# Kernel tuning notes

Measured on AMD Instinct MI355X. Metric: run time of the kernel, lower is better.

## Reference

```python
import jax, jax.numpy as jnp
import numpy as np

D = 2            # stalk dimension d
FD = 3           # final_d = d + 1 (add_lp=True, add_hp=False)
HID = 32         # hidden_channels
N_NODES = 50000
E0 = 200000      # undirected edges; directed edge list has 2*E0 entries (second half reversed)
IN_CH = 128
OUT_CH = 32
N_LAYERS = 2
PSIZE = D * (D + 1) // 2  # cayley param size per edge


def _spectral_normalize(W, iters=20):
    # torch spectral_norm: power iteration with detached u, v; sigma = u^T W v
    u = jnp.full((W.shape[0],), 1.0 / np.sqrt(W.shape[0]), W.dtype)
    def body(_, u):
        v = W.T @ u
        v = v / (jnp.linalg.norm(v) + 1e-12)
        u2 = W @ v
        return u2 / (jnp.linalg.norm(u2) + 1e-12)
    u = jax.lax.fori_loop(0, iters, body, u)
    u = jax.lax.stop_gradient(u)
    v = jax.lax.stop_gradient(W.T @ u)
    v = v / (jnp.linalg.norm(v) + 1e-12)
    return W / (u @ W @ v)


def _cayley(p):
    # p: [E, PSIZE] lower-tri params -> skew A -> orthogonal Q = (I - A)^{-1}(I + A)
    E = p.shape[0]
    r, c = jnp.tril_indices(D)
    M = jnp.zeros((E, D, D), p.dtype).at[:, r, c].set(p)
    A = M - jnp.swapaxes(M, 1, 2)
    I = jnp.eye(D, dtype=p.dtype)
    return jnp.linalg.solve(I[None] - A, I[None] + A)


def setup_inputs() -> dict:
    key = jax.random.key(0)
    ks = jax.random.split(key, 8)
    src = jax.random.randint(ks[0], (E0,), 0, N_NODES)
    dst = jax.random.randint(ks[1], (E0,), 0, N_NODES)
    # symmetric directed edge list; edge j and edge j+E0 are reverses of each other
    edge_index = jnp.concatenate([jnp.stack([src, dst]), jnp.stack([dst, src])], axis=1)
    x = jax.random.normal(ks[2], (N_NODES, IN_CH), jnp.float32)
    s = 0.02
    W1 = jax.random.normal(ks[3], (FD * HID, IN_CH), jnp.float32) * s
    b1 = jnp.zeros((FD * HID,), jnp.float32)
    W2 = jax.random.normal(ks[4], (OUT_CH, FD * HID), jnp.float32) * s
    b2 = jnp.zeros((OUT_CH,), jnp.float32)
    W_left = jnp.tile(jnp.eye(FD, dtype=jnp.float32)[None], (N_LAYERS, 1, 1))  # init eye per torch
    W_right = jax.random.normal(ks[5], (N_LAYERS, HID, HID), jnp.float32) / np.sqrt(HID)
    eps = jnp.zeros((N_LAYERS, FD, 1), jnp.float32)
    W_sheaf = jax.random.normal(ks[6], (N_LAYERS, PSIZE, 2 * FD * HID), jnp.float32) * s
    W_wt = jax.random.normal(ks[7], (N_LAYERS, 1, 2 * FD * HID), jnp.float32) * s
    return {"x": x, "edge_index": edge_index, "W1": W1, "b1": b1, "W2": W2, "b2": b2,
            "W_left": W_left, "W_right": W_right, "eps": eps, "W_sheaf": W_sheaf, "W_wt": W_wt}


def reference(x, edge_index, W1, b1, W2, b2, W_left, W_right, eps, W_sheaf, W_wt):
    N = x.shape[0]
    row, col = edge_index[0], edge_index[1]
    e0 = row.shape[0] // 2
    rev = jnp.concatenate([jnp.arange(e0) + e0, jnp.arange(e0)])  # reverse-edge index
    # lin1 + ELU (dropouts = 0 in eval)
    h = jax.nn.elu(x @ W1.T + b1)                 # [N, FD*HID]
    xc = h.reshape(N * FD, HID)                   # [N*FD, HID]
    x0 = xc
    for layer in range(N_LAYERS):
        # --- sheaf learner + edge weight learner (gather endpoint features) ---
        xn = xc.reshape(N, FD * HID)
        cat = jnp.concatenate([xn[row], xn[col]], axis=-1)   # [2*E0, 2*FD*HID]
        p = jnp.tanh(cat @ W_sheaf[layer].T)                 # sheaf map params [2*E0, PSIZE]
        wdir = jax.nn.sigmoid(cat @ W_wt[layer].T)[:, 0]
        w = wdir * wdir[rev]                                 # symmetric edge weight
        # --- normalized connection (bundle) Laplacian ---
        Q = _cayley(p)                                       # per-edge orthogonal maps
        T = jnp.einsum('eij,eik->ejk', Q, Q[rev])            # transport F_u^T F_v
        w2 = w * w
        deg = jax.ops.segment_sum(w2, row, num_segments=N)
        dinv = jnp.where(deg > 0, jax.lax.rsqrt(jnp.maximum(deg, 1e-30)), 0.0)
        cnorm = w2 * dinv[row] * dinv[col]                   # [2*E0]
        # --- left / right weights (spectral-normalized) ---
        Wl = _spectral_normalize(W_left[layer])
        Wr = _spectral_normalize(W_right[layer])
        y = xc.reshape(N, FD, HID)
        y = jnp.einsum('ef,nfh->neh', Wl, y)                 # mix stalk dims
        y = jnp.einsum('neh,ch->nec', y, Wr)                 # mix channels
        # --- apply block-sparse Laplacian: Lx[u] = x[u] - sum_e c_e B_e x[v] ---
        yv = y[col]                                          # gather  [2*E0, FD, HID]
        tv = jnp.concatenate([jnp.einsum('eij,ejh->eih', T, yv[:, :D]), yv[:, D:]], axis=1)
        agg = jax.ops.segment_sum(cnorm[:, None, None] * tv, row, num_segments=N)
        diag = jnp.where(deg > 0, 1.0, 0.0)[:, None, None]
        z = jax.nn.elu((diag * y - agg).reshape(N * FD, HID))
        # --- epsilon-gated residual ---
        coeff = jnp.tile(1.0 + jnp.tanh(eps[layer]), (N, 1))  # [N*FD, 1]
        x0 = coeff * x0 - z
        xc = x0
    return xc.reshape(N, FD * HID) @ W2.T + b2
```

## Files before the change

kernel.cpp:

```cpp
#include <hip/hip_runtime.h>

#define NN 50000
#define E0 200000
#define E2 400000
#define NGROUPS ((NN + 7) / 8)
#define NCHUNK  ((NN + 255) / 256)
#define NTILES  ((NN + 63) / 64)

typedef __attribute__((ext_vector_type(8))) short short8;
typedef __attribute__((ext_vector_type(4))) float f32x4;

__device__ __forceinline__ float eluf(float x) { return x > 0.0f ? x : expm1f(x); }
__device__ __forceinline__ float sigmoidf(float x) { return 1.0f / (1.0f + expf(-x)); }
__device__ __forceinline__ unsigned rne_bf16(float x) {
    unsigned u = __float_as_uint(x);
    return (u + 0x7fffu + ((u >> 16) & 1u)) >> 16;
}

__global__ __launch_bounds__(256) void k_setup(const float* __restrict__ W1, const float* __restrict__ W2,
                                               const float* __restrict__ Wl_in, const float* __restrict__ Wr_in,
                                               float* __restrict__ Wl_out, float* __restrict__ Wr_out,
                                               unsigned short* __restrict__ w1hi, unsigned short* __restrict__ w1lo,
                                               unsigned short* __restrict__ w2hi, unsigned short* __restrict__ w2lo,
                                               int* __restrict__ cnt, int* __restrict__ fill,
                                               float* __restrict__ deg) {
    __shared__ float W[32 * 33];
    __shared__ float us[32], vs[32], tmp[32];
    __shared__ float scal;
    int t = threadIdx.x;
    if (blockIdx.x < 2) {
        int l = blockIdx.x;
        for (int i = t; i < 1024; i += 256) W[(i >> 5) * 33 + (i & 31)] = Wr_in[l * 1024 + i];
        if (t < 32) us[t] = 0.17677669529663688f;
        __syncthreads();
        for (int it = 0; it < 20; ++it) {
            if (t < 32) { float a = 0; for (int r = 0; r < 32; ++r) a = fmaf(W[r * 33 + t], us[r], a); tmp[t] = a; }
            __syncthreads();
            if (t == 0) { float s = 0; for (int c = 0; c < 32; ++c) s += tmp[c] * tmp[c]; scal = 1.0f / (sqrtf(s) + 1e-12f); }
            __syncthreads();
            if (t < 32) vs[t] = tmp[t] * scal;
            __syncthreads();
            if (t < 32) { float a = 0; for (int c = 0; c < 32; ++c) a = fmaf(W[t * 33 + c], vs[c], a); tmp[t] = a; }
            __syncthreads();
            if (t == 0) { float s = 0; for (int r = 0; r < 32; ++r) s += tmp[r] * tmp[r]; scal = 1.0f / (sqrtf(s) + 1e-12f); }
            __syncthreads();
            if (t < 32) us[t] = tmp[t] * scal;
            __syncthreads();
        }
        if (t < 32) { float a = 0; for (int r = 0; r < 32; ++r) a = fmaf(W[r * 33 + t], us[r], a); tmp[t] = a; }
        __syncthreads();
        if (t == 0) {
            float s = 0; for (int c = 0; c < 32; ++c) s += tmp[c] * tmp[c];
            scal = (sqrtf(s) + 1e-12f) / s;
        }
        __syncthreads();
        for (int i = t; i < 1024; i += 256) Wr_out[l * 1024 + i] = W[(i >> 5) * 33 + (i & 31)] * scal;
        if (t == 0) {
            float M[9];
            for (int i = 0; i < 9; ++i) M[i] = Wl_in[l * 9 + i];
            float u[3] = {0.5773502691896258f, 0.5773502691896258f, 0.5773502691896258f};
            float v[3], u2[3];
            for (int it = 0; it < 20; ++it) {
                float s = 0;
                for (int c = 0; c < 3; ++c) { v[c] = M[c] * u[0] + M[3 + c] * u[1] + M[6 + c] * u[2]; s += v[c] * v[c]; }
                float inv = 1.0f / (sqrtf(s) + 1e-12f);
                for (int c = 0; c < 3; ++c) v[c] *= inv;
                s = 0;
                for (int r = 0; r < 3; ++r) { u2[r] = M[r * 3] * v[0] + M[r * 3 + 1] * v[1] + M[r * 3 + 2] * v[2]; s += u2[r] * u2[r]; }
                inv = 1.0f / (sqrtf(s) + 1e-12f);
                for (int r = 0; r < 3; ++r) u[r] = u2[r] * inv;
            }
            float s = 0;
            for (int c = 0; c < 3; ++c) { v[c] = M[c] * u[0] + M[3 + c] * u[1] + M[6 + c] * u[2]; s += v[c] * v[c]; }
            float inv = (sqrtf(s) + 1e-12f) / s;
            for (int i = 0; i < 9; ++i) Wl_out[l * 9 + i] = M[i] * inv;
        }
    } else {
        int base = (blockIdx.x - 2) * 256 + t;
        int stride = (gridDim.x - 2) * 256;
        for (int i = base; i < 96 * 128; i += stride) {
            float v = W1[i];
            unsigned h = rne_bf16(v);
            w1hi[i] = (unsigned short)h;
            w1lo[i] = (unsigned short)rne_bf16(v - __uint_as_float(h << 16));
        }
        for (int i = base; i < 32 * 96; i += stride) {
            float v = W2[i];
            unsigned h = rne_bf16(v);
            w2hi[i] = (unsigned short)h;
            w2lo[i] = (unsigned short)rne_bf16(v - __uint_as_float(h << 16));
        }
        for (int i = base; i < NN; i += stride) { cnt[i] = 0; fill[i] = 0; deg[i] = 0.0f; }
    }
}

template<int K, int N, bool ELU, bool HIST>
__global__ __launch_bounds__(256) void k_gemm(const float* __restrict__ X,
                                              const unsigned short* __restrict__ Whi,
                                              const unsigned short* __restrict__ Wlo,
                                              const float* __restrict__ bias,
                                              float* __restrict__ out,
                                              const int* __restrict__ row, int* __restrict__ cnt) {
    constexpr int NT = N / 16;
    constexpr int KS = K / 32;
    int tid = threadIdx.x;
    int wave = tid >> 6, lane = tid & 63;
    int quad = lane >> 4, r16 = lane & 15;
    long m = (long)blockIdx.x * 64 + wave * 16 + r16;
    long mc = m < NN ? m : (NN - 1);
    const float* xrow = X + mc * K + quad * 8;
    short8 ah[KS], al[KS];
#pragma unroll
    for (int ks = 0; ks < KS; ++ks) {
        const float4* xp = (const float4*)(xrow + ks * 32);
        float4 p0 = xp[0], p1 = xp[1];
        float xv[8] = {p0.x, p0.y, p0.z, p0.w, p1.x, p1.y, p1.z, p1.w};
#pragma unroll
        for (int j = 0; j < 8; ++j) {
            unsigned h = rne_bf16(xv[j]);
            ah[ks][j] = (short)h;
            al[ks][j] = (short)rne_bf16(xv[j] - __uint_as_float(h << 16));
        }
    }
    f32x4 acc[NT];
#pragma unroll
    for (int t = 0; t < NT; ++t) acc[t] = (f32x4){0.f, 0.f, 0.f, 0.f};
#pragma unroll
    for (int t = 0; t < NT; ++t) {
        int bo = (t * 16 + r16) * K + quad * 8;
#pragma unroll
        for (int ks = 0; ks < KS; ++ks) {
            short8 bh = *(const short8*)&Whi[bo + ks * 32];
            short8 bl = *(const short8*)&Wlo[bo + ks * 32];
            acc[t] = __builtin_amdgcn_mfma_f32_16x16x32_bf16(ah[ks], bh, acc[t], 0, 0, 0);
            acc[t] = __builtin_amdgcn_mfma_f32_16x16x32_bf16(al[ks], bh, acc[t], 0, 0, 0);
            acc[t] = __builtin_amdgcn_mfma_f32_16x16x32_bf16(ah[ks], bl, acc[t], 0, 0, 0);
        }
    }
    long mbase = (long)blockIdx.x * 64 + wave * 16 + quad * 4;
#pragma unroll
    for (int t = 0; t < NT; ++t) {
        float b = bias[t * 16 + r16];
#pragma unroll
        for (int rr = 0; rr < 4; ++rr) {
            long mm = mbase + rr;
            if (mm < NN) {
                float v = acc[t][rr] + b;
                if (ELU) v = eluf(v);
                out[mm * N + t * 16 + r16] = v;
            }
        }
    }
    if (HIST) {
        for (int e = blockIdx.x * 256 + tid; e < E2; e += gridDim.x * 256)
            atomicAdd(&cnt[row[e]], 1);
    }
}

__global__ __launch_bounds__(256) void k_scan1(const int* __restrict__ cnt, int* __restrict__ start,
                                               int* __restrict__ bsum) {
    __shared__ int s[256];
    int b = blockIdx.x, t = threadIdx.x;
    int i = b * 256 + t;
    int v = (i < NN) ? cnt[i] : 0;
    s[t] = v;
    __syncthreads();
    for (int off = 1; off < 256; off <<= 1) {
        int add = (t >= off) ? s[t - off] : 0;
        __syncthreads();
        s[t] += add;
        __syncthreads();
    }
    if (i < NN) start[i] = s[t] - v;
    if (t == 255) bsum[b] = s[t];
}
__global__ __launch_bounds__(256) void k_scan2(const int* __restrict__ bsum, int* __restrict__ bofs, int nb) {
    __shared__ int s[256];
    int t = threadIdx.x;
    int v = (t < nb) ? bsum[t] : 0;
    s[t] = v;
    __syncthreads();
    for (int off = 1; off < 256; off <<= 1) {
        int add = (t >= off) ? s[t - off] : 0;
        __syncthreads();
        s[t] += add;
        __syncthreads();
    }
    if (t < nb) bofs[t] = s[t] - v;
}
__global__ __launch_bounds__(256) void k_fill(const int* __restrict__ row, const int* __restrict__ start,
                                              const int* __restrict__ bofs,
                                              int* __restrict__ fill, int* __restrict__ eslot) {
    int e = blockIdx.x * 256 + threadIdx.x;
    if (e >= E2) return;
    int u = row[e];
    eslot[e] = start[u] + bofs[u >> 8] + atomicAdd(&fill[u], 1);
}

__global__ __launch_bounds__(256) void k_y8(const float* __restrict__ xc,
                                            const float* __restrict__ Wl, const float* __restrict__ Wr,
                                            const float* __restrict__ Wsh, const float* __restrict__ Wwt,
                                            int layer, uint2* __restrict__ yp,
                                            float* __restrict__ aR, float* __restrict__ aC,
                                            float* __restrict__ wR, float* __restrict__ wC,
                                            float* __restrict__ deg) {
    __shared__ float wrs[32 * 33];
    __shared__ float wls[9];
    __shared__ float xcs[8][96];
    __shared__ float ws1[192], wt[192];
    int tid = threadIdx.x;
    int n0 = blockIdx.x * 8;
    if (tid < 8) { int nz = n0 + tid; if (nz < NN) deg[nz] = 0.0f; }
    for (int i = tid; i < 1024; i += 256) wrs[(i >> 5) * 33 + (i & 31)] = Wr[i];
    if (tid < 9) wls[tid] = Wl[tid];
    if (tid < 192) {
        ws1[tid] = Wsh[(layer * 3 + 1) * 192 + tid];
        wt[tid]  = Wwt[layer * 192 + tid];
    }
    for (int i = tid; i < 768; i += 256) {
        int n = n0 + i / 96;
        xcs[i / 96][i % 96] = (n < NN) ? xc[n * 96 + i % 96] : 0.0f;
    }
    __syncthreads();
    int node = tid >> 5, c = tid & 31;
    int n = n0 + node;
    float a1 = 0, a2 = 0, a3 = 0, a4 = 0;
#pragma unroll
    for (int j = 0; j < 3; ++j) {
        int k = j * 32 + c;
        float xv = xcs[node][k];
        a1 = fmaf(xv, ws1[k], a1);
        a2 = fmaf(xv, ws1[96 + k], a2);
        a3 = fmaf(xv, wt[k], a3);
        a4 = fmaf(xv, wt[96 + k], a4);
    }
#pragma unroll
    for (int off = 16; off; off >>= 1) {
        a1 += __shfl_xor(a1, off);
        a2 += __shfl_xor(a2, off);
        a3 += __shfl_xor(a3, off);
        a4 += __shfl_xor(a4, off);
    }
    if (c == 0 && n < NN) { aR[n] = a1; aC[n] = a2; wR[n] = a3; wC[n] = a4; }
    if (n < NN) {
        float t0 = 0, t1 = 0, t2 = 0;
        const float* wr = &wrs[c * 33];
        const float* xr = xcs[node];
#pragma unroll
        for (int h = 0; h < 32; ++h) {
            float w = wr[h];
            t0 = fmaf(xr[h], w, t0);
            t1 = fmaf(xr[32 + h], w, t1);
            t2 = fmaf(xr[64 + h], w, t2);
        }
        float o0 = wls[0] * t0 + wls[1] * t1 + wls[2] * t2;
        float o1 = wls[3] * t0 + wls[4] * t1 + wls[5] * t2;
        float o2 = wls[6] * t0 + wls[7] * t1 + wls[8] * t2;
        yp[n * 32 + c] = make_uint2(rne_bf16(o0) | (rne_bf16(o1) << 16), rne_bf16(o2));
    }
}

__global__ __launch_bounds__(256) void k_coef(const int* __restrict__ row, const int* __restrict__ col,
                                              const int* __restrict__ eslot,
                                              const float* __restrict__ aR, const float* __restrict__ aC,
                                              const float* __restrict__ wR, const float* __restrict__ wC,
                                              float4* __restrict__ meta, float* __restrict__ deg) {
    int e = blockIdx.x * 256 + threadIdx.x;
    if (e >= E0) return;
    int u = row[e], v = col[e];
    float a_e = tanhf(aR[u] + aC[v]);
    float a_r = tanhf(aR[v] + aC[u]);
    float wd_e = sigmoidf(wR[u] + wC[v]);
    float wd_r = sigmoidf(wR[v] + wC[u]);
    float w = wd_e * wd_r;
    float w2 = w * w;
    float ie = 1.0f / (1.0f + a_e * a_e), ir = 1.0f / (1.0f + a_r * a_r);
    float ce = (1.0f - a_e * a_e) * ie, se = 2.0f * a_e * ie;
    float cr = (1.0f - a_r * a_r) * ir, sr = 2.0f * a_r * ir;
    float C = ce * cr + se * sr;
    float S = ce * sr - se * cr;
    meta[eslot[e]]      = make_float4(C,  S, w2, __int_as_float(v));
    meta[eslot[e + E0]] = make_float4(C, -S, w2, __int_as_float(u));
    atomicAdd(&deg[u], w2);
    atomicAdd(&deg[v], w2);
}

__global__ __launch_bounds__(256) void k_dinv(const float* __restrict__ deg, float* __restrict__ dinv) {
    int n = blockIdx.x * 256 + threadIdx.x;
    if (n >= NN) return;
    float d = deg[n];
    dinv[n] = d > 0.0f ? rsqrtf(fmaxf(d, 1e-30f)) : 0.0f;
}

__global__ __launch_bounds__(256) void k_gather(const int* __restrict__ start, const int* __restrict__ bofs,
                                                const int* __restrict__ cnt,
                                                const float4* __restrict__ meta,
                                                const float* __restrict__ dinv,
                                                const uint2* __restrict__ yp,
                                                const float* __restrict__ eps,
                                                int layer, float* __restrict__ xc) {
    int tid = threadIdx.x;
    int node = tid >> 5, c = tid & 31;
    int n = blockIdx.x * 8 + node;
    if (n >= NN) return;
    int s0 = start[n] + bofs[n >> 8], ec = cnt[n];
    float du = dinv[n];
    float acc0 = 0, acc1 = 0, acc2 = 0;
    for (int bs = 0; bs < ec; bs += 32) {
        int nb2 = min(32, ec - bs);
        float CC = 0, SS = 0, cnl = 0;
        int vj = 0;
        if (c < nb2) {
            float4 mt = meta[s0 + bs + c];
            vj = __float_as_int(mt.w);
            cnl = mt.z * du * dinv[vj];
            CC = cnl * mt.x;
            SS = cnl * mt.y;
        }
        for (int j = 0; j < nb2; ++j) {
            float Cj = __shfl(CC, j, 32);
            float Sj = __shfl(SS, j, 32);
            float cj = __shfl(cnl, j, 32);
            int v = __shfl(vj, j, 32);
            uint2 uy = yp[v * 32 + c];
            float y0 = __uint_as_float(uy.x << 16);
            float y1 = __uint_as_float(uy.x & 0xffff0000u);
            float y2 = __uint_as_float(uy.y << 16);
            acc0 = fmaf(Cj, y0, acc0);
            acc0 = fmaf(-Sj, y1, acc0);
            acc1 = fmaf(Sj, y0, acc1);
            acc1 = fmaf(Cj, y1, acc1);
            acc2 = fmaf(cj, y2, acc2);
        }
    }
    float diag = du > 0.0f ? 1.0f : 0.0f;
    uint2 uy = yp[n * 32 + c];
    float oy0 = __uint_as_float(uy.x << 16);
    float oy1 = __uint_as_float(uy.x & 0xffff0000u);
    float oy2 = __uint_as_float(uy.y << 16);
    float c0 = 1.0f + tanhf(eps[layer * 3 + 0]);
    float c1 = 1.0f + tanhf(eps[layer * 3 + 1]);
    float c2 = 1.0f + tanhf(eps[layer * 3 + 2]);
    int base = n * 96 + c;
    float z0 = eluf(diag * oy0 - acc0);
    float z1 = eluf(diag * oy1 - acc1);
    float z2 = eluf(diag * oy2 - acc2);
    xc[base]      = c0 * xc[base]      - z0;
    xc[base + 32] = c1 * xc[base + 32] - z1;
    xc[base + 64] = c2 * xc[base + 64] - z2;
}

extern "C" void kernel_launch(void* const* d_in, const int* in_sizes, int n_in,
                              void* d_out, int out_size, void* d_ws, size_t ws_size,
                              hipStream_t stream) {
    const float* x     = (const float*)d_in[0];
    const int*   ei    = (const int*)d_in[1];
    const float* W1    = (const float*)d_in[2];
    const float* b1    = (const float*)d_in[3];
    const float* W2    = (const float*)d_in[4];
    const float* b2    = (const float*)d_in[5];
    const float* Wl    = (const float*)d_in[6];
    const float* Wr    = (const float*)d_in[7];
    const float* eps   = (const float*)d_in[8];
    const float* Wsh   = (const float*)d_in[9];
    const float* Wwt   = (const float*)d_in[10];
    float* out = (float*)d_out;
    const int* row = ei;
    const int* col = ei + E2;

    char* pc = (char*)d_ws;
    float* xc    = (float*)pc;          pc += (size_t)NN * 96 * 4;
    float4* meta = (float4*)pc;         pc += (size_t)E2 * 16;
    uint2* yp    = (uint2*)pc;          pc += (size_t)NN * 32 * 8;
    float* aR    = (float*)pc;          pc += (size_t)NN * 4;
    float* aC    = (float*)pc;          pc += (size_t)NN * 4;
    float* wRp   = (float*)pc;          pc += (size_t)NN * 4;
    float* wCp   = (float*)pc;          pc += (size_t)NN * 4;
    float* deg   = (float*)pc;          pc += (size_t)NN * 4;
    float* dinv  = (float*)pc;          pc += (size_t)NN * 4;
    float* Wl_n  = (float*)pc;          pc += 32 * 4;
    float* Wr_n  = (float*)pc;          pc += 2048 * 4;
    int* cnt     = (int*)pc;            pc += (size_t)NN * 4;
    int* start   = (int*)pc;            pc += (size_t)NN * 4;
    int* fill    = (int*)pc;            pc += (size_t)NN * 4;
    int* eslot   = (int*)pc;            pc += (size_t)E2 * 4;
    int* bsum    = (int*)pc;            pc += 256 * 4;
    int* bofs    = (int*)pc;            pc += 256 * 4;
    unsigned short* w1hi = (unsigned short*)pc; pc += 96 * 128 * 2;
    unsigned short* w1lo = (unsigned short*)pc; pc += 96 * 128 * 2;
    unsigned short* w2hi = (unsigned short*)pc; pc += 32 * 96 * 2;
    unsigned short* w2lo = (unsigned short*)pc; pc += 32 * 96 * 2;

    const int EB = (E2 + 255) / 256;

    k_setup<<<66, 256, 0, stream>>>(W1, W2, Wl, Wr, Wl_n, Wr_n,
                                    w1hi, w1lo, w2hi, w2lo, cnt, fill, deg);
    k_gemm<128, 96, true, true><<<NTILES, 256, 0, stream>>>(x, w1hi, w1lo, b1, xc, row, cnt);
    k_scan1<<<NCHUNK, 256, 0, stream>>>(cnt, start, bsum);
    k_scan2<<<1, 256, 0, stream>>>(bsum, bofs, NCHUNK);
    k_fill<<<EB, 256, 0, stream>>>(row, start, bofs, fill, eslot);
    for (int l = 0; l < 2; ++l) {
        k_y8<<<NGROUPS, 256, 0, stream>>>(xc, Wl_n + l * 9, Wr_n + l * 1024, Wsh, Wwt, l,
                                          yp, aR, aC, wRp, wCp, deg);
        k_coef<<<(E0 + 255) / 256, 256, 0, stream>>>(row, col, eslot, aR, aC, wRp, wCp, meta, deg);
        k_dinv<<<NCHUNK, 256, 0, stream>>>(deg, dinv);
        k_gather<<<NGROUPS, 256, 0, stream>>>(start, bofs, cnt, meta, dinv, yp, eps, l, xc);
    }
    k_gemm<96, 32, false, false><<<NTILES, 256, 0, stream>>>(xc, w2hi, w2lo, b2, out, nullptr, nullptr);
}
```

Measured before the change: 367.4 us.

## Fuse weight bf16 split into GEMM via LDS and inline dinv into gather

The hi/lo bf16 split of W1 and W2 now happens inside each GEMM block and is staged in padded shared memory, so the global precomputed weight buffers and their setup pass go away. The edge-histogram atomics move to the start of the first GEMM kernel. The separate k_dinv kernel is removed and the gather computes rsqrt of the degree inline for both endpoints. These changes drop kernel launches and global weight reloads, at the cost of every GEMM block redoing the weight conversion, extra LDS use, and repeated rsqrt work per edge.

After: 361.1 us. Within noise of the previous version (-1.7%).

```diff
diff --git a/kernel.cpp b/kernel.cpp
--- a/kernel.cpp
+++ b/kernel.cpp
@@ -17,11 +17,8 @@
     return (u + 0x7fffu + ((u >> 16) & 1u)) >> 16;
 }
 
-__global__ __launch_bounds__(256) void k_setup(const float* __restrict__ W1, const float* __restrict__ W2,
-                                               const float* __restrict__ Wl_in, const float* __restrict__ Wr_in,
+__global__ __launch_bounds__(256) void k_setup(const float* __restrict__ Wl_in, const float* __restrict__ Wr_in,
                                                float* __restrict__ Wl_out, float* __restrict__ Wr_out,
-                                               unsigned short* __restrict__ w1hi, unsigned short* __restrict__ w1lo,
-                                               unsigned short* __restrict__ w2hi, unsigned short* __restrict__ w2lo,
                                                int* __restrict__ cnt, int* __restrict__ fill,
                                                float* __restrict__ deg) {
     __shared__ float W[32 * 33];
@@ -78,32 +75,34 @@
     } else {
         int base = (blockIdx.x - 2) * 256 + t;
         int stride = (gridDim.x - 2) * 256;
-        for (int i = base; i < 96 * 128; i += stride) {
-            float v = W1[i];
-            unsigned h = rne_bf16(v);
-            w1hi[i] = (unsigned short)h;
-            w1lo[i] = (unsigned short)rne_bf16(v - __uint_as_float(h << 16));
-        }
-        for (int i = base; i < 32 * 96; i += stride) {
-            float v = W2[i];
-            unsigned h = rne_bf16(v);
-            w2hi[i] = (unsigned short)h;
-            w2lo[i] = (unsigned short)rne_bf16(v - __uint_as_float(h << 16));
-        }
         for (int i = base; i < NN; i += stride) { cnt[i] = 0; fill[i] = 0; deg[i] = 0.0f; }
     }
 }
 
 template<int K, int N, bool ELU, bool HIST>
 __global__ __launch_bounds__(256) void k_gemm(const float* __restrict__ X,
-                                              const unsigned short* __restrict__ Whi,
-                                              const unsigned short* __restrict__ Wlo,
+                                              const float* __restrict__ W,
                                               const float* __restrict__ bias,
                                               float* __restrict__ out,
                                               const int* __restrict__ row, int* __restrict__ cnt) {
+    constexpr int KP = K + 8;
     constexpr int NT = N / 16;
     constexpr int KS = K / 32;
+    __shared__ __align__(16) unsigned short whi[N * KP];
+    __shared__ __align__(16) unsigned short wlo[N * KP];
     int tid = threadIdx.x;
+    if (HIST) {
+        for (int e = blockIdx.x * 256 + tid; e < E2; e += gridDim.x * 256)
+            atomicAdd(&cnt[row[e]], 1);
+    }
+    for (int i = tid; i < N * K; i += 256) {
+        float v = W[i];
+        int r = i / K, c = i % K;
+        unsigned h = rne_bf16(v);
+        whi[r * KP + c] = (unsigned short)h;
+        wlo[r * KP + c] = (unsigned short)rne_bf16(v - __uint_as_float(h << 16));
+    }
+    __syncthreads();
     int wave = tid >> 6, lane = tid & 63;
     int quad = lane >> 4, r16 = lane & 15;
     long m = (long)blockIdx.x * 64 + wave * 16 + r16;
@@ -122,38 +121,29 @@
             al[ks][j] = (short)rne_bf16(xv[j] - __uint_as_float(h << 16));
         }
     }
-    f32x4 acc[NT];
-#pragma unroll
-    for (int t = 0; t < NT; ++t) acc[t] = (f32x4){0.f, 0.f, 0.f, 0.f};
+    long mbase = (long)blockIdx.x * 64 + wave * 16 + quad * 4;
 #pragma unroll
     for (int t = 0; t < NT; ++t) {
-        int bo = (t * 16 + r16) * K + quad * 8;
+        f32x4 acc = (f32x4){0.f, 0.f, 0.f, 0.f};
 #pragma unroll
         for (int ks = 0; ks < KS; ++ks) {
-            short8 bh = *(const short8*)&Whi[bo + ks * 32];
-            short8 bl = *(const short8*)&Wlo[bo + ks * 32];
-            acc[t] = __builtin_amdgcn_mfma_f32_16x16x32_bf16(ah[ks], bh, acc[t], 0, 0, 0);
-            acc[t] = __builtin_amdgcn_mfma_f32_16x16x32_bf16(al[ks], bh, acc[t], 0, 0, 0);
-            acc[t] = __builtin_amdgcn_mfma_f32_16x16x32_bf16(ah[ks], bl, acc[t], 0, 0, 0);
-        }
-    }
-    long mbase = (long)blockIdx.x * 64 + wave * 16 + quad * 4;
-#pragma unroll
-    for (int t = 0; t < NT; ++t) {
+            int ro = (t * 16 + r16) * KP + ks * 32 + quad * 8;
+            short8 bh = *(const short8*)&whi[ro];
+            short8 bl = *(const short8*)&wlo[ro];
+            acc = __builtin_amdgcn_mfma_f32_16x16x32_bf16(ah[ks], bh, acc, 0, 0, 0);
+            acc = __builtin_amdgcn_mfma_f32_16x16x32_bf16(al[ks], bh, acc, 0, 0, 0);
+            acc = __builtin_amdgcn_mfma_f32_16x16x32_bf16(ah[ks], bl, acc, 0, 0, 0);
+        }
         float b = bias[t * 16 + r16];
 #pragma unroll
         for (int rr = 0; rr < 4; ++rr) {
             long mm = mbase + rr;
             if (mm < NN) {
-                float v = acc[t][rr] + b;
+                float v = acc[rr] + b;
                 if (ELU) v = eluf(v);
                 out[mm * N + t * 16 + r16] = v;
             }
         }
-    }
-    if (HIST) {
-        for (int e = blockIdx.x * 256 + tid; e < E2; e += gridDim.x * 256)
-            atomicAdd(&cnt[row[e]], 1);
     }
 }
 
@@ -285,17 +275,10 @@
     atomicAdd(&deg[v], w2);
 }
 
-__global__ __launch_bounds__(256) void k_dinv(const float* __restrict__ deg, float* __restrict__ dinv) {
-    int n = blockIdx.x * 256 + threadIdx.x;
-    if (n >= NN) return;
-    float d = deg[n];
-    dinv[n] = d > 0.0f ? rsqrtf(fmaxf(d, 1e-30f)) : 0.0f;
-}
-
 __global__ __launch_bounds__(256) void k_gather(const int* __restrict__ start, const int* __restrict__ bofs,
                                                 const int* __restrict__ cnt,
                                                 const float4* __restrict__ meta,
-                                                const float* __restrict__ dinv,
+                                                const float* __restrict__ deg,
                                                 const uint2* __restrict__ yp,
                                                 const float* __restrict__ eps,
                                                 int layer, float* __restrict__ xc) {
@@ -304,7 +287,8 @@
     int n = blockIdx.x * 8 + node;
     if (n >= NN) return;
     int s0 = start[n] + bofs[n >> 8], ec = cnt[n];
-    float du = dinv[n];
+    float dn = deg[n];
+    float du = dn > 0.0f ? rsqrtf(fmaxf(dn, 1e-30f)) : 0.0f;
     float acc0 = 0, acc1 = 0, acc2 = 0;
     for (int bs = 0; bs < ec; bs += 32) {
         int nb2 = min(32, ec - bs);
@@ -313,7 +297,9 @@
         if (c < nb2) {
             float4 mt = meta[s0 + bs + c];
             vj = __float_as_int(mt.w);
-            cnl = mt.z * du * dinv[vj];
+            float dv = deg[vj];
+            float dvi = dv > 0.0f ? rsqrtf(fmaxf(dv, 1e-30f)) : 0.0f;
+            cnl = mt.z * du * dvi;
             CC = cnl * mt.x;
             SS = cnl * mt.y;
         }
@@ -333,7 +319,7 @@
             acc2 = fmaf(cj, y2, acc2);
         }
     }
-    float diag = du > 0.0f ? 1.0f : 0.0f;
+    float diag = dn > 0.0f ? 1.0f : 0.0f;
     uint2 uy = yp[n * 32 + c];
     float oy0 = __uint_as_float(uy.x << 16);
     float oy1 = __uint_as_float(uy.x & 0xffff0000u);
@@ -377,7 +363,6 @@
     float* wRp   = (float*)pc;          pc += (size_t)NN * 4;
     float* wCp   = (float*)pc;          pc += (size_t)NN * 4;
     float* deg   = (float*)pc;          pc += (size_t)NN * 4;
-    float* dinv  = (float*)pc;          pc += (size_t)NN * 4;
     float* Wl_n  = (float*)pc;          pc += 32 * 4;
     float* Wr_n  = (float*)pc;          pc += 2048 * 4;
     int* cnt     = (int*)pc;            pc += (size_t)NN * 4;
@@ -386,16 +371,11 @@
     int* eslot   = (int*)pc;            pc += (size_t)E2 * 4;
     int* bsum    = (int*)pc;            pc += 256 * 4;
     int* bofs    = (int*)pc;            pc += 256 * 4;
-    unsigned short* w1hi = (unsigned short*)pc; pc += 96 * 128 * 2;
-    unsigned short* w1lo = (unsigned short*)pc; pc += 96 * 128 * 2;
-    unsigned short* w2hi = (unsigned short*)pc; pc += 32 * 96 * 2;
-    unsigned short* w2lo = (unsigned short*)pc; pc += 32 * 96 * 2;
 
     const int EB = (E2 + 255) / 256;
 
-    k_setup<<<66, 256, 0, stream>>>(W1, W2, Wl, Wr, Wl_n, Wr_n,
-                                    w1hi, w1lo, w2hi, w2lo, cnt, fill, deg);
-    k_gemm<128, 96, true, true><<<NTILES, 256, 0, stream>>>(x, w1hi, w1lo, b1, xc, row, cnt);
+    k_setup<<<34, 256, 0, stream>>>(Wl, Wr, Wl_n, Wr_n, cnt, fill, deg);
+    k_gemm<128, 96, true, true><<<NTILES, 256, 0, stream>>>(x, W1, b1, xc, row, cnt);
     k_scan1<<<NCHUNK, 256, 0, stream>>>(cnt, start, bsum);
     k_scan2<<<1, 256, 0, stream>>>(bsum, bofs, NCHUNK);
     k_fill<<<EB, 256, 0, stream>>>(row, start, bofs, fill, eslot);
@@ -403,8 +383,7 @@
         k_y8<<<NGROUPS, 256, 0, stream>>>(xc, Wl_n + l * 9, Wr_n + l * 1024, Wsh, Wwt, l,
                                           yp, aR, aC, wRp, wCp, deg);
         k_coef<<<(E0 + 255) / 256, 256, 0, stream>>>(row, col, eslot, aR, aC, wRp, wCp, meta, deg);
-        k_dinv<<<NCHUNK, 256, 0, stream>>>(deg, dinv);
-        k_gather<<<NGROUPS, 256, 0, stream>>>(start, bofs, cnt, meta, dinv, yp, eps, l, xc);
-    }
-    k_gemm<96, 32, false, false><<<NTILES, 256, 0, stream>>>(xc, w2hi, w2lo, b2, out, nullptr, nullptr);
-}
+        k_gather<<<NGROUPS, 256, 0, stream>>>(start, bofs, cnt, meta, deg, yp, eps, l, xc);
+    }
+    k_gemm<96, 32, false, false><<<NTILES, 256, 0, stream>>>(xc, W2, b2, out, nullptr, nullptr);
+}
```
